# Performance work log

Measured on AMD Instinct MI355X. Metric: run time of the kernel, lower is better.

## Reference

```python
import jax, jax.numpy as jnp
import numpy as np

M, K, N = 8192, 4096, 4096

def setup_inputs() -> dict:
    key = jax.random.key(0)
    k1, k2, k3, k4, k5, k6 = jax.random.split(key, 6)
    # quantized activations (per-token symmetric int8)
    x_q = jax.random.randint(k1, (M, K), -128, 128, dtype=jnp.int32).astype(jnp.int8)
    # quantized weight (asymmetric per-output-channel): w_fp16 = scale_weight * (w_q + zp_weight)
    weight = jax.random.randint(k2, (N, K), -128, 128, dtype=jnp.int32).astype(jnp.int8)
    scale_input = (jax.random.uniform(k3, (M,), jnp.float32) * 0.009 + 0.001).astype(jnp.float16)
    scale_weight = (jax.random.uniform(k4, (N,), jnp.float32) * 0.009 + 0.001).astype(jnp.float16)
    zp_weight = jax.random.randint(k5, (N,), 100, 156, dtype=jnp.int32).astype(jnp.int16)
    bias = (jax.random.normal(k6, (N,), jnp.float32) * 0.01).astype(jnp.float16)
    # per-row sum of quantized activations (needed for zero-point correction)
    sum_input = jnp.sum(x_q.astype(jnp.int32), axis=-1).astype(jnp.float32)
    return {
        "input": x_q,
        "weight": weight,
        "bias": bias,
        "scale_input": scale_input,
        "scale_weight": scale_weight,
        "sum_input": sum_input,
        "zp_weight": zp_weight,
    }

def reference(input, weight, bias, scale_input, scale_weight, sum_input, zp_weight):
    acc = jnp.matmul(input.astype(jnp.int32), weight.astype(jnp.int32).T)
    # asymmetric weight zero-point correction: + zp_n * sum_k(x_q[m, k])
    corr = sum_input[:, None] * zp_weight.astype(jnp.float32)[None, :]
    # fused dequant epilogue: per-row activation scale * per-col weight scale, + bias
    scale = scale_input.astype(jnp.float32)[:, None] * scale_weight.astype(jnp.float32)[None, :]
    out = (acc.astype(jnp.float32) + corr) * scale + bias.astype(jnp.float32)[None, :]
    return out.astype(jnp.float16)
```

## Files before the change

### kernel.cpp

```cpp
#include <hip/hip_runtime.h>
#include <hip/hip_bf16.h>
#include <stdint.h>


#define BM 256
#define BN 128
#define BK 128

typedef __attribute__((ext_vector_type(4))) int int32x4;
typedef __attribute__((ext_vector_type(16))) int int32x16;

__device__ __forceinline__ void async_copy16(const uint8_t* g, uint8_t* l) {
  __builtin_amdgcn_global_load_lds(
      (const __attribute__((address_space(1))) uint32_t*)(const void*)g,
      (__attribute__((address_space(3))) uint32_t*)l,
      16, 0, 0);
}

__global__ __launch_bounds__(256) void pack_kernel(
    const int* __restrict__ A, const int* __restrict__ B,
    uint8_t* __restrict__ A8, uint8_t* __restrict__ B8,
    int nA4, int nTot4) {
  int t = blockIdx.x * blockDim.x + threadIdx.x;
  if (t >= nTot4) return;
  const int32x4* src;
  uint32_t* dst;
  if (t < nA4) {
    src = (const int32x4*)A + t;
    dst = (uint32_t*)A8 + t;
  } else {
    int u = t - nA4;
    src = (const int32x4*)B + u;
    dst = (uint32_t*)B8 + u;
  }
  int32x4 v = __builtin_nontemporal_load(src);
  *dst = (uint32_t)(v.x & 255) | ((uint32_t)(v.y & 255) << 8) |
         ((uint32_t)(v.z & 255) << 16) | ((uint32_t)(v.w & 255) << 24);
}

__global__ __launch_bounds__(256, 2) void w8a8_gemm(
    const uint8_t* __restrict__ A8, const uint8_t* __restrict__ B8,
    const float* __restrict__ bias,
    const float* __restrict__ s_in,
    const float* __restrict__ s_w,
    const float* __restrict__ sum_in,
    const int* __restrict__ zp_w,
    float* __restrict__ out,
    int M, int N, int K) {
  __shared__ uint8_t As[BM * BK];
  __shared__ uint8_t Bs[BN * BK];

  const int tid = threadIdx.x;
  const int bm = blockIdx.y, bn = blockIdx.x;
  const int row0 = bm * BM, col0 = bn * BN;
  const int wave = tid >> 6, lane = tid & 63;
  const int m32 = lane & 31, half = lane >> 5;
  const int wm = wave * 64;
  const size_t sK = (size_t)K;

  const int row_s = tid >> 3;
  const int cg = (tid & 7) ^ ((tid >> 4) & 7);
  const int ldst = tid * 16;

  int32x16 acc[2][4] = {};

  for (int k0 = 0; k0 < K; k0 += BK) {
#pragma unroll
    for (int p = 0; p < 8; ++p)
      async_copy16(A8 + (size_t)(row0 + p * 32 + row_s) * sK + k0 + cg * 16,
                   &As[p * 4096 + ldst]);
#pragma unroll
    for (int p = 0; p < 4; ++p)
      async_copy16(B8 + (size_t)(col0 + p * 32 + row_s) * sK + k0 + cg * 16,
                   &Bs[p * 4096 + ldst]);
    __syncthreads();

    const int swzr = (m32 >> 1) & 7;
#pragma unroll
    for (int ks = 0; ks < 4; ++ks) {
      const int gran = ((ks * 2 + half) ^ swzr) * 16;
      int32x4 afrag[2], bfrag[4];
#pragma unroll
      for (int i = 0; i < 2; ++i)
        afrag[i] = *(const int32x4*)&As[(wm + i * 32 + m32) * BK + gran];
#pragma unroll
      for (int j = 0; j < 4; ++j)
        bfrag[j] = *(const int32x4*)&Bs[(j * 32 + m32) * BK + gran];
#pragma unroll
      for (int i = 0; i < 2; ++i)
#pragma unroll
        for (int j = 0; j < 4; ++j)
          acc[i][j] = __builtin_amdgcn_mfma_i32_32x32x32_i8(
              afrag[i], bfrag[j], acc[i][j], 0, 0, 0);
    }
    __syncthreads();
  }

  float swj[4], zpj[4], bj[4];
#pragma unroll
  for (int j = 0; j < 4; ++j) {
    int gc = col0 + j * 32 + m32;
    swj[j] = s_w[gc];
    zpj[j] = (float)zp_w[gc];
    bj[j] = bias[gc];
  }
#pragma unroll
  for (int i = 0; i < 2; ++i) {
#pragma unroll
    for (int reg = 0; reg < 16; ++reg) {
      int gr = row0 + wm + i * 32 + (reg & 3) + 8 * (reg >> 2) + 4 * half;
      float siv = s_in[gr];
      float suv = sum_in[gr];
      float* orow = out + (size_t)gr * N + col0 + m32;
#pragma unroll
      for (int j = 0; j < 4; ++j) {
        float v = ((float)acc[i][j][reg] + suv * zpj[j]) * (siv * swj[j]) + bj[j];
        __builtin_nontemporal_store(v, &orow[j * 32]);
      }
    }
  }
}

__global__ __launch_bounds__(256) void w8a8_gemm_fallback(
    const int* __restrict__ A32, const int* __restrict__ B32,
    const float* __restrict__ bias,
    const float* __restrict__ s_in,
    const float* __restrict__ s_w,
    const float* __restrict__ sum_in,
    const int* __restrict__ zp_w,
    float* __restrict__ out,
    int M, int N, int K) {
  __shared__ uint8_t As[128 * 64];
  __shared__ uint8_t Bs[128 * 64];
  const int tid = threadIdx.x;
  const int bm = blockIdx.y, bn = blockIdx.x;
  const int row0 = bm * 128, col0 = bn * 128;
  const int wave = tid >> 6, lane = tid & 63;
  const int quad = lane >> 4, r = lane & 15;
  const int wm = (wave >> 1) * 64, wn = (wave & 1) * 64;
  const int lin = tid * 16;
  const int srow = lin >> 6;
  const int scol = lin & 63;
  const size_t sK = (size_t)K;
  int32x4 acc[4][4] = {};
  for (int k0 = 0; k0 < K; k0 += 64) {
#pragma unroll
    for (int c = 0; c < 2; ++c) {
      const int* ag = A32 + (size_t)(row0 + srow + c * 64) * sK + k0 + scol;
      const int* bg = B32 + (size_t)(col0 + srow + c * 64) * sK + k0 + scol;
      int32x4 pa, pb;
#pragma unroll
      for (int q = 0; q < 4; ++q) {
        int4 va = ((const int4*)ag)[q];
        int4 vb = ((const int4*)bg)[q];
        pa[q] = (int)((uint32_t)(va.x & 255) | ((uint32_t)(va.y & 255) << 8) |
                      ((uint32_t)(va.z & 255) << 16) | ((uint32_t)(va.w & 255) << 24));
        pb[q] = (int)((uint32_t)(vb.x & 255) | ((uint32_t)(vb.y & 255) << 8) |
                      ((uint32_t)(vb.z & 255) << 16) | ((uint32_t)(vb.w & 255) << 24));
      }
      *(int32x4*)&As[lin + c * 4096] = pa;
      *(int32x4*)&Bs[lin + c * 4096] = pb;
    }
    __syncthreads();
    int32x4 afrag[4], bfrag[4];
#pragma unroll
    for (int i = 0; i < 4; ++i)
      afrag[i] = *(const int32x4*)&As[(wm + i * 16 + r) * 64 + quad * 16];
#pragma unroll
    for (int j = 0; j < 4; ++j)
      bfrag[j] = *(const int32x4*)&Bs[(wn + j * 16 + r) * 64 + quad * 16];
#pragma unroll
    for (int i = 0; i < 4; ++i)
#pragma unroll
      for (int j = 0; j < 4; ++j)
        acc[i][j] = __builtin_amdgcn_mfma_i32_16x16x64_i8(afrag[i], bfrag[j],
                                                          acc[i][j], 0, 0, 0);
    __syncthreads();
  }
  float swj[4], zpj[4], bj[4];
#pragma unroll
  for (int j = 0; j < 4; ++j) {
    int gc = col0 + wn + j * 16 + r;
    swj[j] = s_w[gc];
    zpj[j] = (float)zp_w[gc];
    bj[j] = bias[gc];
  }
#pragma unroll
  for (int i = 0; i < 4; ++i) {
#pragma unroll
    for (int t = 0; t < 4; ++t) {
      int gr = row0 + wm + i * 16 + quad * 4 + t;
      float siv = s_in[gr];
      float suv = sum_in[gr];
      float* orow = out + (size_t)gr * N + col0 + wn + r;
#pragma unroll
      for (int j = 0; j < 4; ++j) {
        float v = ((float)acc[i][j][t] + suv * zpj[j]) * (siv * swj[j]) + bj[j];
        orow[j * 16] = v;
      }
    }
  }
}

extern "C" void kernel_launch(void* const* d_in, const int* in_sizes, int n_in,
                              void* d_out, int out_size, void* d_ws, size_t ws_size,
                              hipStream_t stream) {
  const int* x_q = (const int*)d_in[0];
  const int* w_q = (const int*)d_in[1];
  const float* bias = (const float*)d_in[2];
  const float* s_in = (const float*)d_in[3];
  const float* s_w = (const float*)d_in[4];
  const float* sum_in = (const float*)d_in[5];
  const int* zp_w = (const int*)d_in[6];
  float* out = (float*)d_out;

  const int M = in_sizes[3];
  const int N = in_sizes[2];
  const int K = in_sizes[0] / M;

  const size_t needA = (size_t)M * K;
  const size_t needB = (size_t)N * K;

  if (ws_size >= needA + needB) {
    uint8_t* A8 = (uint8_t*)d_ws;
    uint8_t* B8 = A8 + needA;
    const int nA4 = (int)(needA / 4);
    const int nTot4 = (int)((needA + needB) / 4);
    pack_kernel<<<(nTot4 + 255) / 256, 256, 0, stream>>>(x_q, w_q, A8, B8,
                                                         nA4, nTot4);
    dim3 grid(N / BN, M / BM), block(256);
    w8a8_gemm<<<grid, block, 0, stream>>>(A8, B8, bias, s_in, s_w, sum_in,
                                          zp_w, out, M, N, K);
  } else {
    dim3 grid(N / 128, M / 128), block(256);
    w8a8_gemm_fallback<<<grid, block, 0, stream>>>(x_q, w_q, bias, s_in, s_w,
                                                   sum_in, zp_w, out, M, N, K);
  }
}
```

Baseline: 396.8 us.

## Double-buffer LDS tiles with 256x256 blocks, 8 waves, and XCD-aware block remap

The GEMM kernel moves to 256x256 output tiles computed by 512 threads (8 waves, each owning 128x64). LDS is double-buffered, and the next-next K tile is prefetched asynchronously with manual vmcnt waits, so loads overlap MFMA work instead of being serialized by barriers. Block indices are remapped across the 8 XCDs to improve L2 locality, MFMA sections raise wave priority, and the pack kernel becomes a capped grid-stride loop. The kernel now needs 128KB of LDS per block, which limits occupancy and adds register pressure.

```diff
diff --git a/kernel.cpp b/kernel.cpp
--- a/kernel.cpp
+++ b/kernel.cpp
@@ -1,10 +1,9 @@
 #include <hip/hip_runtime.h>
-#include <hip/hip_bf16.h>
 #include <stdint.h>
 
 
 #define BM 256
-#define BN 128
+#define BN 256
 #define BK 128
 
 typedef __attribute__((ext_vector_type(4))) int int32x4;
@@ -21,24 +20,36 @@
     const int* __restrict__ A, const int* __restrict__ B,
     uint8_t* __restrict__ A8, uint8_t* __restrict__ B8,
     int nA4, int nTot4) {
-  int t = blockIdx.x * blockDim.x + threadIdx.x;
-  if (t >= nTot4) return;
-  const int32x4* src;
-  uint32_t* dst;
-  if (t < nA4) {
-    src = (const int32x4*)A + t;
-    dst = (uint32_t*)A8 + t;
-  } else {
-    int u = t - nA4;
-    src = (const int32x4*)B + u;
-    dst = (uint32_t*)B8 + u;
-  }
-  int32x4 v = __builtin_nontemporal_load(src);
-  *dst = (uint32_t)(v.x & 255) | ((uint32_t)(v.y & 255) << 8) |
-         ((uint32_t)(v.z & 255) << 16) | ((uint32_t)(v.w & 255) << 24);
-}
-
-__global__ __launch_bounds__(256, 2) void w8a8_gemm(
+  const int stride = gridDim.x * blockDim.x;
+  for (int t = blockIdx.x * blockDim.x + threadIdx.x; t < nTot4; t += stride) {
+    const int32x4* src;
+    uint32_t* dst;
+    if (t < nA4) {
+      src = (const int32x4*)A + t;
+      dst = (uint32_t*)A8 + t;
+    } else {
+      int u = t - nA4;
+      src = (const int32x4*)B + u;
+      dst = (uint32_t*)B8 + u;
+    }
+    int32x4 v = __builtin_nontemporal_load(src);
+    *dst = (uint32_t)(v.x & 255) | ((uint32_t)(v.y & 255) << 8) |
+           ((uint32_t)(v.z & 255) << 16) | ((uint32_t)(v.w & 255) << 24);
+  }
+}
+
+__device__ __forceinline__ void stage_tile(
+    const uint8_t* Ab, const uint8_t* Bb, size_t sK, int k0,
+    uint8_t* AsBuf, uint8_t* BsBuf, int ldst) {
+#pragma unroll
+  for (int p = 0; p < 4; ++p)
+    async_copy16(Ab + (size_t)(p * 64) * sK + k0, AsBuf + p * 8192 + ldst);
+#pragma unroll
+  for (int p = 0; p < 4; ++p)
+    async_copy16(Bb + (size_t)(p * 64) * sK + k0, BsBuf + p * 8192 + ldst);
+}
+
+__global__ __launch_bounds__(512, 2) void w8a8_gemm(
     const uint8_t* __restrict__ A8, const uint8_t* __restrict__ B8,
     const float* __restrict__ bias,
     const float* __restrict__ s_in,
@@ -47,73 +58,94 @@
     const int* __restrict__ zp_w,
     float* __restrict__ out,
     int M, int N, int K) {
-  __shared__ uint8_t As[BM * BK];
-  __shared__ uint8_t Bs[BN * BK];
+  __shared__ uint8_t As[2][BM * BK];
+  __shared__ uint8_t Bs[2][BN * BK];
 
   const int tid = threadIdx.x;
-  const int bm = blockIdx.y, bn = blockIdx.x;
+  const int nbn = N / BN;
+  int wgs = blockIdx.x;
+  if ((gridDim.x & 7) == 0) {
+    const int q = gridDim.x >> 3;
+    wgs = (blockIdx.x & 7) * q + (blockIdx.x >> 3);
+  }
+  const int bm = wgs / nbn, bn = wgs % nbn;
   const int row0 = bm * BM, col0 = bn * BN;
+
   const int wave = tid >> 6, lane = tid & 63;
   const int m32 = lane & 31, half = lane >> 5;
-  const int wm = wave * 64;
+  const int wm = (wave >> 2) * 128;
+  const int wn = (wave & 3) * 64;
   const size_t sK = (size_t)K;
 
   const int row_s = tid >> 3;
   const int cg = (tid & 7) ^ ((tid >> 4) & 7);
   const int ldst = tid * 16;
 
-  int32x16 acc[2][4] = {};
-
-  for (int k0 = 0; k0 < K; k0 += BK) {
-#pragma unroll
-    for (int p = 0; p < 8; ++p)
-      async_copy16(A8 + (size_t)(row0 + p * 32 + row_s) * sK + k0 + cg * 16,
-                   &As[p * 4096 + ldst]);
-#pragma unroll
-    for (int p = 0; p < 4; ++p)
-      async_copy16(B8 + (size_t)(col0 + p * 32 + row_s) * sK + k0 + cg * 16,
-                   &Bs[p * 4096 + ldst]);
-    __syncthreads();
-
-    const int swzr = (m32 >> 1) & 7;
+  const uint8_t* Ab = A8 + (size_t)(row0 + row_s) * sK + cg * 16;
+  const uint8_t* Bb = B8 + (size_t)(col0 + row_s) * sK + cg * 16;
+
+  int32x16 acc[4][2] = {};
+
+  const int NT = K / BK;
+  stage_tile(Ab, Bb, sK, 0, &As[0][0], &Bs[0][0], ldst);
+  if (NT > 1) stage_tile(Ab, Bb, sK, BK, &As[1][0], &Bs[1][0], ldst);
+
+  int cur = 0;
+  const int swzr = (m32 >> 1) & 7;
+  for (int kt = 0; kt < NT; ++kt) {
+    if (kt + 1 < NT) {
+      asm volatile("s_waitcnt vmcnt(8)" ::: "memory");
+    } else {
+      asm volatile("s_waitcnt vmcnt(0)" ::: "memory");
+    }
+    __builtin_amdgcn_s_barrier();
+
+    const uint8_t* Ac = &As[cur][0];
+    const uint8_t* Bc = &Bs[cur][0];
+    __builtin_amdgcn_s_setprio(1);
 #pragma unroll
     for (int ks = 0; ks < 4; ++ks) {
       const int gran = ((ks * 2 + half) ^ swzr) * 16;
-      int32x4 afrag[2], bfrag[4];
-#pragma unroll
-      for (int i = 0; i < 2; ++i)
-        afrag[i] = *(const int32x4*)&As[(wm + i * 32 + m32) * BK + gran];
-#pragma unroll
-      for (int j = 0; j < 4; ++j)
-        bfrag[j] = *(const int32x4*)&Bs[(j * 32 + m32) * BK + gran];
-#pragma unroll
-      for (int i = 0; i < 2; ++i)
-#pragma unroll
-        for (int j = 0; j < 4; ++j)
+      int32x4 afrag[4], bfrag[2];
+#pragma unroll
+      for (int i = 0; i < 4; ++i)
+        afrag[i] = *(const int32x4*)&Ac[(wm + i * 32 + m32) * BK + gran];
+#pragma unroll
+      for (int j = 0; j < 2; ++j)
+        bfrag[j] = *(const int32x4*)&Bc[(wn + j * 32 + m32) * BK + gran];
+#pragma unroll
+      for (int i = 0; i < 4; ++i)
+#pragma unroll
+        for (int j = 0; j < 2; ++j)
           acc[i][j] = __builtin_amdgcn_mfma_i32_32x32x32_i8(
               afrag[i], bfrag[j], acc[i][j], 0, 0, 0);
     }
-    __syncthreads();
-  }
-
-  float swj[4], zpj[4], bj[4];
-#pragma unroll
-  for (int j = 0; j < 4; ++j) {
-    int gc = col0 + j * 32 + m32;
+    __builtin_amdgcn_s_setprio(0);
+    asm volatile("s_waitcnt lgkmcnt(0)" ::: "memory");
+    __builtin_amdgcn_s_barrier();
+    if (kt + 2 < NT)
+      stage_tile(Ab, Bb, sK, (kt + 2) * BK, &As[cur][0], &Bs[cur][0], ldst);
+    cur ^= 1;
+  }
+
+  float swj[2], zpj[2], bj[2];
+#pragma unroll
+  for (int j = 0; j < 2; ++j) {
+    int gc = col0 + wn + j * 32 + m32;
     swj[j] = s_w[gc];
     zpj[j] = (float)zp_w[gc];
     bj[j] = bias[gc];
   }
 #pragma unroll
-  for (int i = 0; i < 2; ++i) {
+  for (int i = 0; i < 4; ++i) {
 #pragma unroll
     for (int reg = 0; reg < 16; ++reg) {
       int gr = row0 + wm + i * 32 + (reg & 3) + 8 * (reg >> 2) + 4 * half;
       float siv = s_in[gr];
       float suv = sum_in[gr];
-      float* orow = out + (size_t)gr * N + col0 + m32;
-#pragma unroll
-      for (int j = 0; j < 4; ++j) {
+      float* orow = out + (size_t)gr * N + col0 + wn + m32;
+#pragma unroll
+      for (int j = 0; j < 2; ++j) {
         float v = ((float)acc[i][j][reg] + suv * zpj[j]) * (siv * swj[j]) + bj[j];
         __builtin_nontemporal_store(v, &orow[j * 32]);
       }
@@ -221,14 +253,16 @@
   const size_t needA = (size_t)M * K;
   const size_t needB = (size_t)N * K;
 
-  if (ws_size >= needA + needB) {
+  if (ws_size >= needA + needB && (M % BM) == 0 && (N % BN) == 0 &&
+      (K % BK) == 0) {
     uint8_t* A8 = (uint8_t*)d_ws;
     uint8_t* B8 = A8 + needA;
     const int nA4 = (int)(needA / 4);
     const int nTot4 = (int)((needA + needB) / 4);
-    pack_kernel<<<(nTot4 + 255) / 256, 256, 0, stream>>>(x_q, w_q, A8, B8,
-                                                         nA4, nTot4);
-    dim3 grid(N / BN, M / BM), block(256);
+    int nblk = (nTot4 + 255) / 256;
+    if (nblk > 2048) nblk = 2048;
+    pack_kernel<<<nblk, 256, 0, stream>>>(x_q, w_q, A8, B8, nA4, nTot4);
+    dim3 grid((M / BM) * (N / BN)), block(512);
     w8a8_gemm<<<grid, block, 0, stream>>>(A8, B8, bias, s_in, s_w, sum_in,
                                           zp_w, out, M, N, K);
   } else {
```

Measured after the change: 405.6 us. 2.2% more time.

## Pre-pack A into MFMA fragment layout and load A directly to registers

Applied to the files above, without the earlier changes.

The pack kernel now writes the activation matrix in a blocked layout that matches the MFMA 32x32x32 operand fragments, so each lane can read its A fragments straight from global memory with 16-byte loads. The A tile no longer goes through LDS, which halves shared-memory traffic and lowers LDS usage per block. The pack kernel also becomes grid-stride with a capped block count. In exchange, A reads now have global-load latency inside the k-loop with no LDS staging to hide it. The fast path now also requires a power-of-two K and tile-divisible sizes.

```diff
diff --git a/kernel.cpp b/kernel.cpp
--- a/kernel.cpp
+++ b/kernel.cpp
@@ -1,5 +1,4 @@
 #include <hip/hip_runtime.h>
-#include <hip/hip_bf16.h>
 #include <stdint.h>
 
 
@@ -20,22 +19,31 @@
 __global__ __launch_bounds__(256) void pack_kernel(
     const int* __restrict__ A, const int* __restrict__ B,
     uint8_t* __restrict__ A8, uint8_t* __restrict__ B8,
-    int nA4, int nTot4) {
-  int t = blockIdx.x * blockDim.x + threadIdx.x;
-  if (t >= nTot4) return;
-  const int32x4* src;
-  uint32_t* dst;
-  if (t < nA4) {
-    src = (const int32x4*)A + t;
-    dst = (uint32_t*)A8 + t;
-  } else {
-    int u = t - nA4;
-    src = (const int32x4*)B + u;
-    dst = (uint32_t*)B8 + u;
-  }
-  int32x4 v = __builtin_nontemporal_load(src);
-  *dst = (uint32_t)(v.x & 255) | ((uint32_t)(v.y & 255) << 8) |
-         ((uint32_t)(v.z & 255) << 16) | ((uint32_t)(v.w & 255) << 24);
+    int nA4, int nTot4, int kc32, int shift ) {
+  const int stride = gridDim.x * blockDim.x;
+  const int k4mask = (1 << shift) - 1;
+  for (int t = blockIdx.x * blockDim.x + threadIdx.x; t < nTot4; t += stride) {
+    const int32x4* src = (t < nA4) ? ((const int32x4*)A + t)
+                                   : ((const int32x4*)B + (t - nA4));
+    int32x4 x = __builtin_nontemporal_load(src);
+    uint32_t v = (uint32_t)(x.x & 255) | ((uint32_t)(x.y & 255) << 8) |
+                 ((uint32_t)(x.z & 255) << 16) | ((uint32_t)(x.w & 255) << 24);
+    if (t < nA4) {
+      const int r = t >> shift, k = (t & k4mask) << 2;
+      const int p = r >> 5, m32 = r & 31;
+      const int c = k >> 5, half = (k >> 4) & 1, slot = (k >> 2) & 3;
+      ((uint32_t*)A8)[(size_t)(((p * kc32 + c) * 2 + half) * 32 + m32) * 4 + slot] = v;
+    } else {
+      ((uint32_t*)B8)[t - nA4] = v;
+    }
+  }
+}
+
+__device__ __forceinline__ void stage_B(const uint8_t* Bb, size_t sK, int k0,
+                                        uint8_t* BsBuf, int ldst) {
+#pragma unroll
+  for (int p = 0; p < 4; ++p)
+    async_copy16(Bb + (size_t)(p * 32) * sK + k0, BsBuf + p * 4096 + ldst);
 }
 
 __global__ __launch_bounds__(256, 2) void w8a8_gemm(
@@ -47,42 +55,49 @@
     const int* __restrict__ zp_w,
     float* __restrict__ out,
     int M, int N, int K) {
-  __shared__ uint8_t As[BM * BK];
   __shared__ uint8_t Bs[BN * BK];
 
   const int tid = threadIdx.x;
   const int bm = blockIdx.y, bn = blockIdx.x;
   const int row0 = bm * BM, col0 = bn * BN;
+
   const int wave = tid >> 6, lane = tid & 63;
   const int m32 = lane & 31, half = lane >> 5;
   const int wm = wave * 64;
   const size_t sK = (size_t)K;
-
+  const int kc32 = K >> 5;
+
+  const int cg = (tid & 7) ^ ((tid >> 4) & 7);
   const int row_s = tid >> 3;
-  const int cg = (tid & 7) ^ ((tid >> 4) & 7);
   const int ldst = tid * 16;
+  const uint8_t* Bb = B8 + (size_t)(col0 + row_s) * sK + cg * 16;
+
+  size_t paOff[2];
+#pragma unroll
+  for (int i = 0; i < 2; ++i)
+    paOff[i] = ((size_t)((row0 >> 5) + wave * 2 + i) * kc32) << 10;
+  const uint8_t* Apl = A8 + (lane << 4);
 
   int32x16 acc[2][4] = {};
 
-  for (int k0 = 0; k0 < K; k0 += BK) {
-#pragma unroll
-    for (int p = 0; p < 8; ++p)
-      async_copy16(A8 + (size_t)(row0 + p * 32 + row_s) * sK + k0 + cg * 16,
-                   &As[p * 4096 + ldst]);
-#pragma unroll
-    for (int p = 0; p < 4; ++p)
-      async_copy16(B8 + (size_t)(col0 + p * 32 + row_s) * sK + k0 + cg * 16,
-                   &Bs[p * 4096 + ldst]);
-    __syncthreads();
-
-    const int swzr = (m32 >> 1) & 7;
+  const int swzr = (m32 >> 1) & 7;
+  const int NT = K / BK;
+  for (int kt = 0; kt < NT; ++kt) {
+    const int k0 = kt * BK;
+    stage_B(Bb, sK, k0, Bs, ldst);
+    int32x4 afr[4][2];
+    const size_t kcOff = ((size_t)(k0 >> 5)) << 10;
+#pragma unroll
+    for (int ks = 0; ks < 4; ++ks)
+#pragma unroll
+      for (int i = 0; i < 2; ++i)
+        afr[ks][i] = *(const int32x4*)(Apl + paOff[i] + kcOff + ((size_t)ks << 10));
+    __syncthreads();
+
 #pragma unroll
     for (int ks = 0; ks < 4; ++ks) {
       const int gran = ((ks * 2 + half) ^ swzr) * 16;
-      int32x4 afrag[2], bfrag[4];
-#pragma unroll
-      for (int i = 0; i < 2; ++i)
-        afrag[i] = *(const int32x4*)&As[(wm + i * 32 + m32) * BK + gran];
+      int32x4 bfrag[4];
 #pragma unroll
       for (int j = 0; j < 4; ++j)
         bfrag[j] = *(const int32x4*)&Bs[(j * 32 + m32) * BK + gran];
@@ -91,7 +106,7 @@
 #pragma unroll
         for (int j = 0; j < 4; ++j)
           acc[i][j] = __builtin_amdgcn_mfma_i32_32x32x32_i8(
-              afrag[i], bfrag[j], acc[i][j], 0, 0, 0);
+              afr[ks][i], bfrag[j], acc[i][j], 0, 0, 0);
     }
     __syncthreads();
   }
@@ -220,14 +235,20 @@
 
   const size_t needA = (size_t)M * K;
   const size_t needB = (size_t)N * K;
-
-  if (ws_size >= needA + needB) {
+  const bool kPow2 = (K & (K - 1)) == 0;
+
+  if (ws_size >= needA + needB && (M % BM) == 0 && (N % BN) == 0 &&
+      (K % BK) == 0 && kPow2) {
     uint8_t* A8 = (uint8_t*)d_ws;
     uint8_t* B8 = A8 + needA;
     const int nA4 = (int)(needA / 4);
     const int nTot4 = (int)((needA + needB) / 4);
-    pack_kernel<<<(nTot4 + 255) / 256, 256, 0, stream>>>(x_q, w_q, A8, B8,
-                                                         nA4, nTot4);
+    int shift = 0;
+    while ((1 << (shift + 1)) <= (K >> 2)) ++shift;
+    int nblk = (nTot4 + 255) / 256;
+    if (nblk > 2048) nblk = 2048;
+    pack_kernel<<<nblk, 256, 0, stream>>>(x_q, w_q, A8, B8, nA4, nTot4,
+                                          K >> 5, shift);
     dim3 grid(N / BN, M / BM), block(256);
     w8a8_gemm<<<grid, block, 0, stream>>>(A8, B8, bias, s_in, s_w, sum_in,
                                           zp_w, out, M, N, K);
```

Result: slower. 406.4 us (+2.4%).
